# Kernel tuning notes

Measured on AMD Instinct MI355X. Metric: run time of the kernel, lower is better.

Reference implementation:

```python
import jax, jax.numpy as jnp
import numpy as np

H = 256          # hidden_size
L = 2            # num_layers
K = 4            # khops
R = 128          # relation_num
N_NODES = 20000
N_EDGES = 160000
N_LG_EDGES = 640000


def setup_inputs() -> dict:
    key = jax.random.key(0)
    ks = iter(jax.random.split(key, 40))
    def nrm(shape, s=1.0):
        return jax.random.normal(next(ks), shape, dtype=jnp.float32) * s
    w = 1.0 / float(np.sqrt(H))
    return {
        "x": nrm((N_NODES, H)),
        "edge_feat": jax.random.randint(next(ks), (N_EDGES,), 0, R),
        "edge_index_g": jax.random.randint(next(ks), (2, N_EDGES), 0, N_NODES),
        "edge_index_lg": jax.random.randint(next(ks), (2, N_LG_EDGES), 0, N_EDGES),
        "rel_embed": nrm((R, H)),
        # per-layer, per-core (0=node update, 1=edge update) parameter stacks
        "w_self": nrm((L, 2, H, H), w), "b_self": jnp.zeros((L, 2, H), jnp.float32),
        "w_khop": nrm((L, 2, K, H, H), w), "b_khop": jnp.zeros((L, 2, K, H), jnp.float32),
        "w_fuse": nrm((L, 2, H, H), w), "b_fuse": jnp.zeros((L, 2, H), jnp.float32),
        "w_ff1": nrm((L, 2, H, 4 * H), w), "b_ff1": jnp.zeros((L, 2, 4 * H), jnp.float32),
        "w_ff2": nrm((L, 2, 4 * H, H), 1.0 / float(np.sqrt(4 * H))), "b_ff2": jnp.zeros((L, 2, H), jnp.float32),
        "ln1_g": jnp.ones((L, 2, H), jnp.float32), "ln1_b": jnp.zeros((L, 2, H), jnp.float32),
        "ln2_g": jnp.ones((L, 2, H), jnp.float32), "ln2_b": jnp.zeros((L, 2, H), jnp.float32),
    }


def _layernorm(x, g, b, eps=1e-5):
    m = jnp.mean(x, axis=-1, keepdims=True)
    v = jnp.var(x, axis=-1, keepdims=True)
    return (x - m) * jax.lax.rsqrt(v + eps) * g + b


def _core(p, src, dst, x, fused):
    """LGNNCore.forward (eval mode, dropout never applied in core)."""
    (ws, bs, wk, bk, wf, bf, w1, b1, w2, b2, g1, c1, g2, c2) = p
    n = x.shape[0]
    prev = x @ ws + bs
    # k-hop copy_src + sum aggregation, each hop gets its own linear
    z = x
    kh = jnp.zeros_like(prev)
    for i in range(wk.shape[0]):
        z = jax.ops.segment_sum(z[src], dst, num_segments=n)
        kh = kh + z @ wk[i] + bk[i]
    edge = fused @ wf + bf
    out = jax.nn.gelu(prev + kh + edge, approximate=False)
    out = _layernorm(x + out, g1, c1)
    ffn = jax.nn.gelu(out @ w1 + b1, approximate=False) @ w2 + b2
    return _layernorm(out + ffn, g2, c2)


def reference(x, edge_feat, edge_index_g, edge_index_lg, rel_embed,
              w_self, b_self, w_khop, b_khop, w_fuse, b_fuse,
              w_ff1, b_ff1, w_ff2, b_ff2, ln1_g, ln1_b, ln2_g, ln2_b):
    lg_x = rel_embed[edge_feat]                       # [n_edges, H]
    src_g, dst_g = edge_index_g[0], edge_index_g[1]
    src_l, dst_l = edge_index_lg[0], edge_index_lg[1]
    n_nodes = x.shape[0]
    for l in range(w_self.shape[0]):
        def pick(c):
            return (w_self[l, c], b_self[l, c], w_khop[l, c], b_khop[l, c],
                    w_fuse[l, c], b_fuse[l, c], w_ff1[l, c], b_ff1[l, c],
                    w_ff2[l, c], b_ff2[l, c], ln1_g[l, c], ln1_b[l, c],
                    ln2_g[l, c], ln2_b[l, c])
        # pmpd @ lg_x : scatter each edge feature to both of its endpoints
        fused_nodes = (jax.ops.segment_sum(lg_x, src_g, num_segments=n_nodes)
                       + jax.ops.segment_sum(lg_x, dst_g, num_segments=n_nodes))
        # pmpd^T @ x : gather both endpoint node features per edge
        fused_edges = x[src_g] + x[dst_g]
        new_x = _core(pick(0), src_g, dst_g, x, fused_nodes)
        new_lg_x = _core(pick(1), src_l, dst_l, lg_x, fused_edges)
        x, lg_x = new_x, new_lg_x
    return x, lg_x
```

## Files before the change

### kernel.cpp

```cpp
#include <hip/hip_runtime.h>

typedef __bf16 bf16;
typedef __attribute__((ext_vector_type(8))) __bf16 bf16x8;
typedef __attribute__((ext_vector_type(4))) __bf16 bf16x4;
typedef __attribute__((ext_vector_type(4))) float f32x4;

#define HD 256
#define GEMM_GELU 2

__device__ __forceinline__ float gelu_f(float x) {
  float x2 = x * x;
  float u = 1.5957691216057308f * x * fmaf(0.044715f, x2, 1.0f);
  float e = __expf(-u);
  return x / (1.0f + e);
}

__device__ __forceinline__ void gload_lds16(const void* g, void* l) {
  __builtin_amdgcn_global_load_lds(
      (const __attribute__((address_space(1))) unsigned int*)g,
      (__attribute__((address_space(3))) unsigned int*)l, 16, 0, 0);
}

__global__ __launch_bounds__(256) void gemm_k(
    const bf16* __restrict__ A, const bf16* __restrict__ Wt,
    const float* __restrict__ bias, bf16* __restrict__ C,
    int M, int Kd, int lda, int ldc, int flags)
{
  __shared__ __align__(16) bf16 sA[2][128 * 64];
  __shared__ __align__(16) bf16 sB[2][128 * 64];
  const int t = threadIdx.x;
  const int lane = t & 63, w = t >> 6;
  const int n0 = blockIdx.x * 128, m0 = blockIdx.y * 128;
  const int wr = w >> 1, wc = w & 1;
  const int lm = lane & 15, quad = lane >> 4;

  const int rowl = lane >> 3;
  const int gcl = (lane & 7) ^ rowl;
  const bool full = (m0 + 128 <= M);

  const char* pa = (const char*)(A + (size_t)(m0 + w * 32 + rowl) * lda) + gcl * 16;
  const char* pb = (const char*)(Wt + (size_t)(n0 + w * 32 + rowl) * Kd) + gcl * 16;
  const size_t stepA = (size_t)8 * lda * 2;
  const size_t stepB = (size_t)8 * Kd * 2;

  f32x4 acc[4][4];
#pragma unroll
  for (int i = 0; i < 4; i++)
#pragma unroll
    for (int j = 0; j < 4; j++)
#pragma unroll
      for (int r = 0; r < 4; r++) acc[i][j][r] = 0.f;

  const int nk = Kd >> 6;

  auto stage = [&](bf16* SA, bf16* SB, int kt) {
    size_t ko = (size_t)kt * 128;
#pragma unroll
    for (int i = 0; i < 4; i++)
      gload_lds16(pa + i * stepA + ko, SA + w * 2048 + i * 512);
#pragma unroll
    for (int i = 0; i < 4; i++)
      gload_lds16(pb + i * stepB + ko, SB + w * 2048 + i * 512);
  };

  auto compute = [&](const bf16* SA, const bf16* SB) {
#pragma unroll
    for (int s = 0; s < 2; s++) {
      const int soff = ((s * 4 + quad) ^ (lm & 7)) * 8;
      bf16x8 af[4], bv[4];
#pragma unroll
      for (int i = 0; i < 4; i++) af[i] = *(const bf16x8*)(SA + (wr * 64 + i * 16 + lm) * 64 + soff);
#pragma unroll
      for (int j = 0; j < 4; j++) bv[j] = *(const bf16x8*)(SB + (wc * 64 + j * 16 + lm) * 64 + soff);
#pragma unroll
      for (int i = 0; i < 4; i++)
#pragma unroll
        for (int j = 0; j < 4; j++)
          acc[i][j] = __builtin_amdgcn_mfma_f32_16x16x32_bf16(bv[j], af[i], acc[i][j], 0, 0, 0);
    }
  };

  if (full) {
    stage(sA[0], sB[0], 0);
    for (int kt = 0; kt < nk; ++kt) {
      int nxt = kt + 1;
      if (nxt < nk) {
        stage(sA[nxt & 1], sB[nxt & 1], nxt);
        asm volatile("s_waitcnt vmcnt(8)" ::: "memory");
      } else {
        asm volatile("s_waitcnt vmcnt(0)" ::: "memory");
      }
      __builtin_amdgcn_s_barrier();
      asm volatile("" ::: "memory");
      compute(sA[kt & 1], sB[kt & 1]);
      __builtin_amdgcn_s_barrier();
      asm volatile("" ::: "memory");
    }
  } else {
    for (int kt = 0; kt < nk; ++kt) {
      size_t ko = (size_t)kt * 128;
#pragma unroll
      for (int c = 0; c < 4; c++) {
        int sid = t + c * 256;
        int row = sid >> 3, sc = sid & 7;
        int gc = sc ^ (row & 7);
        int gr = m0 + row;
        bf16x8 va;
#pragma unroll
        for (int q = 0; q < 8; q++) va[q] = (bf16)0.f;
        if (gr < M) va = *(const bf16x8*)((const char*)(A + (size_t)gr * lda) + ko + gc * 16);
        *(bf16x8*)(sA[0] + row * 64 + sc * 8) = va;
      }
#pragma unroll
      for (int i = 0; i < 4; i++)
        gload_lds16(pb + i * stepB + ko, sB[0] + w * 2048 + i * 512);
      __syncthreads();
      compute(sA[0], sB[0]);
      __syncthreads();
    }
  }

  float4 bia[4];
#pragma unroll
  for (int j = 0; j < 4; j++)
    bia[j] = *(const float4*)(bias + n0 + wc * 64 + j * 16 + quad * 4);
#pragma unroll
  for (int i = 0; i < 4; i++) {
    int gr = m0 + wr * 64 + i * 16 + lm;
    if (gr < M) {
      bf16* crow = C + (size_t)gr * ldc;
#pragma unroll
      for (int j = 0; j < 4; j++) {
        int gc = n0 + wc * 64 + j * 16 + quad * 4;
        float v0 = acc[i][j][0] + bia[j].x;
        float v1 = acc[i][j][1] + bia[j].y;
        float v2 = acc[i][j][2] + bia[j].z;
        float v3 = acc[i][j][3] + bia[j].w;
        if (flags & GEMM_GELU) {
          v0 = gelu_f(v0); v1 = gelu_f(v1); v2 = gelu_f(v2); v3 = gelu_f(v3);
        }
        bf16x4 o = {(bf16)v0, (bf16)v1, (bf16)v2, (bf16)v3};
        *(bf16x4*)(crow + gc) = o;
      }
    }
  }
}

__global__ __launch_bounds__(256) void segsum_k(
    const int* __restrict__ offs, const int* __restrict__ cols,
    const bf16* __restrict__ in, int ldin, bf16* __restrict__ out, int ldout, int nseg)
{
  int wid = threadIdx.x >> 6, lane = threadIdx.x & 63;
  int seg = blockIdx.x * 4 + wid;
  if (seg >= nseg) return;
  int b = offs[seg], e = offs[seg + 1];
  float a0 = 0.f, a1 = 0.f, a2 = 0.f, a3 = 0.f;
  for (int i = b; i < e; i++) {
    int c = cols[i];
    bf16x4 v = *(const bf16x4*)(in + (size_t)c * ldin + lane * 4);
    a0 += (float)v.x; a1 += (float)v.y; a2 += (float)v.z; a3 += (float)v.w;
  }
  bf16x4 o = {(bf16)a0, (bf16)a1, (bf16)a2, (bf16)a3};
  *(bf16x4*)(out + (size_t)seg * ldout + lane * 4) = o;
}

__global__ __launch_bounds__(256) void ln_k(
    const bf16* __restrict__ X, int ldx, const bf16* __restrict__ A,
    const float* __restrict__ gam, const float* __restrict__ bet,
    bf16* __restrict__ outb, float* __restrict__ outf, int M, int apply_gelu)
{
  int wid = threadIdx.x >> 6, lane = threadIdx.x & 63;
  int row = blockIdx.x * 4 + wid;
  if (row >= M) return;
  size_t xbase = (size_t)row * ldx + lane * 4;
  size_t abase = (size_t)row * HD + lane * 4;
  bf16x4 xv = *(const bf16x4*)(X + xbase);
  bf16x4 av = *(const bf16x4*)(A + abase);
  float s0, s1, s2, s3;
  if (apply_gelu) {
    s0 = (float)xv.x + gelu_f((float)av.x);
    s1 = (float)xv.y + gelu_f((float)av.y);
    s2 = (float)xv.z + gelu_f((float)av.z);
    s3 = (float)xv.w + gelu_f((float)av.w);
  } else {
    s0 = (float)xv.x + (float)av.x;
    s1 = (float)xv.y + (float)av.y;
    s2 = (float)xv.z + (float)av.z;
    s3 = (float)xv.w + (float)av.w;
  }
  float sum = s0 + s1 + s2 + s3;
#pragma unroll
  for (int o = 32; o; o >>= 1) sum += __shfl_xor(sum, o, 64);
  float mean = sum * (1.0f / 256.0f);
  float d0 = s0 - mean, d1 = s1 - mean, d2 = s2 - mean, d3 = s3 - mean;
  float vs = d0 * d0 + d1 * d1 + d2 * d2 + d3 * d3;
#pragma unroll
  for (int o = 32; o; o >>= 1) vs += __shfl_xor(vs, o, 64);
  float rstd = rsqrtf(vs * (1.0f / 256.0f) + 1e-5f);
  float4 g = *(const float4*)(gam + lane * 4);
  float4 bb = *(const float4*)(bet + lane * 4);
  float y0 = d0 * rstd * g.x + bb.x;
  float y1 = d1 * rstd * g.y + bb.y;
  float y2 = d2 * rstd * g.z + bb.z;
  float y3 = d3 * rstd * g.w + bb.w;
  if (outb) {
    bf16x4 o = {(bf16)y0, (bf16)y1, (bf16)y2, (bf16)y3};
    *(bf16x4*)(outb + xbase) = o;
  }
  if (outf) {
    float4 o = {y0, y1, y2, y3};
    *(float4*)(outf + abase) = o;
  }
}

__global__ __launch_bounds__(256) void gather_rel_k(
    const int* __restrict__ feat, const float* __restrict__ rel,
    bf16* __restrict__ out, int ldout, int NE)
{
  int wid = threadIdx.x >> 6, lane = threadIdx.x & 63;
  int e = blockIdx.x * 4 + wid;
  if (e >= NE) return;
  int f = feat[e];
  float4 v = *(const float4*)(rel + (size_t)f * HD + lane * 4);
  bf16x4 o = {(bf16)v.x, (bf16)v.y, (bf16)v.z, (bf16)v.w};
  *(bf16x4*)(out + (size_t)e * ldout + lane * 4) = o;
}

__global__ __launch_bounds__(256) void gather2_k(
    const int* __restrict__ src, const int* __restrict__ dst,
    const bf16* __restrict__ x, int ldx, bf16* __restrict__ out, int ldout, int NE)
{
  int wid = threadIdx.x >> 6, lane = threadIdx.x & 63;
  int e = blockIdx.x * 4 + wid;
  if (e >= NE) return;
  int s = src[e], d = dst[e];
  bf16x4 a = *(const bf16x4*)(x + (size_t)s * ldx + lane * 4);
  bf16x4 b = *(const bf16x4*)(x + (size_t)d * ldx + lane * 4);
  bf16x4 o = {(bf16)((float)a.x + (float)b.x), (bf16)((float)a.y + (float)b.y),
              (bf16)((float)a.z + (float)b.z), (bf16)((float)a.w + (float)b.w)};
  *(bf16x4*)(out + (size_t)e * ldout + lane * 4) = o;
}

__global__ __launch_bounds__(256) void f2b_k(const float* __restrict__ in,
                                             bf16* __restrict__ out, int ldout, int M) {
  int wid = threadIdx.x >> 6, lane = threadIdx.x & 63;
  int row = blockIdx.x * 4 + wid;
  if (row >= M) return;
  float4 v = *(const float4*)(in + (size_t)row * HD + lane * 4);
  bf16x4 o = {(bf16)v.x, (bf16)v.y, (bf16)v.z, (bf16)v.w};
  *(bf16x4*)(out + (size_t)row * ldout + lane * 4) = o;
}

__global__ __launch_bounds__(256) void wtrans_k(const float* __restrict__ in, bf16* __restrict__ out,
                                                int Kd, int Nd) {
  size_t moff = (size_t)blockIdx.y * Kd * Nd;
  int id = blockIdx.x * 256 + threadIdx.x;
  if (id >= Kd * Nd) return;
  int n = id / Kd, k = id - n * Kd;
  out[moff + id] = (bf16)in[moff + (size_t)k * Nd + n];
}

__global__ __launch_bounds__(256) void wcat_k(const float* __restrict__ ws, const float* __restrict__ wk,
                                              const float* __restrict__ wf, bf16* __restrict__ out,
                                              int KH, int CW) {
  int mi = blockIdx.y;
  int id = blockIdx.x * 256 + threadIdx.x;
  if (id >= HD * CW) return;
  int n = id / CW, k = id - n * CW;
  int s = k >> 8, kk = k & 255;
  float v;
  if (s == 0)       v = ws[((size_t)mi * HD + kk) * HD + n];
  else if (s <= KH) v = wk[(((size_t)mi * KH + (s - 1)) * HD + kk) * HD + n];
  else              v = wf[((size_t)mi * HD + kk) * HD + n];
  out[(size_t)mi * HD * CW + id] = (bf16)v;
}

__global__ __launch_bounds__(256) void bcat_k(const float* __restrict__ bs, const float* __restrict__ bk,
                                              const float* __restrict__ bf, float* __restrict__ out, int KH) {
  int mi = blockIdx.x, n = threadIdx.x;
  float v = bs[(size_t)mi * HD + n] + bf[(size_t)mi * HD + n];
  for (int i = 0; i < KH; i++) v += bk[((size_t)mi * KH + i) * HD + n];
  out[(size_t)mi * HD + n] = v;
}

__global__ __launch_bounds__(256) void count_k(const int* __restrict__ keys, int n, int* __restrict__ cnt) {
  int i = blockIdx.x * 256 + threadIdx.x;
  if (i < n) atomicAdd(&cnt[keys[i]], 1);
}
__global__ __launch_bounds__(256) void scan1_k(const int* __restrict__ in, int* __restrict__ out,
                                               int* __restrict__ bsum, int n) {
  __shared__ int sh[256];
  int t = threadIdx.x;
  int i0 = blockIdx.x * 1024 + t * 4;
  int v0 = (i0 < n) ? in[i0] : 0;
  int v1 = (i0 + 1 < n) ? in[i0 + 1] : 0;
  int v2 = (i0 + 2 < n) ? in[i0 + 2] : 0;
  int v3 = (i0 + 3 < n) ? in[i0 + 3] : 0;
  int tsum = v0 + v1 + v2 + v3;
  sh[t] = tsum;
  __syncthreads();
  for (int o = 1; o < 256; o <<= 1) {
    int x = (t >= o) ? sh[t - o] : 0;
    __syncthreads();
    sh[t] += x;
    __syncthreads();
  }
  int e0 = sh[t] - tsum;
  if (t == 255) bsum[blockIdx.x] = sh[255];
  if (i0 < n) out[i0] = e0;
  e0 += v0;
  if (i0 + 1 < n) out[i0 + 1] = e0;
  e0 += v1;
  if (i0 + 2 < n) out[i0 + 2] = e0;
  e0 += v2;
  if (i0 + 3 < n) out[i0 + 3] = e0;
}
__global__ void scan2_k(int* bsum, int nb, int* total) {
  if (threadIdx.x == 0 && blockIdx.x == 0) {
    int acc = 0;
    for (int i = 0; i < nb; i++) { int v = bsum[i]; bsum[i] = acc; acc += v; }
    *total = acc;
  }
}
__global__ __launch_bounds__(256) void scan3_k(int* out, const int* bsum, int n) {
  int i = blockIdx.x * 256 + threadIdx.x;
  if (i < n) out[i] += bsum[i >> 10];
}
__global__ __launch_bounds__(256) void fill_k(const int* __restrict__ keys, const int* __restrict__ vals,
                                              int n, int modE, int* __restrict__ cursor, int* __restrict__ cols) {
  int i = blockIdx.x * 256 + threadIdx.x;
  if (i >= n) return;
  int pos = atomicAdd(&cursor[keys[i]], 1);
  cols[pos] = vals ? vals[i] : (i < modE ? i : i - modE);
}

extern "C" void kernel_launch(void* const* d_in, const int* in_sizes, int n_in,
                              void* d_out, int out_size, void* d_ws, size_t ws_size,
                              hipStream_t stream)
{
  const float* x_in      = (const float*)d_in[0];
  const int*   edge_feat = (const int*)d_in[1];
  const int*   eig       = (const int*)d_in[2];
  const int*   eil       = (const int*)d_in[3];
  const float* rel       = (const float*)d_in[4];
  const float* w_self = (const float*)d_in[5];
  const float* b_self = (const float*)d_in[6];
  const float* w_khop = (const float*)d_in[7];
  const float* b_khop = (const float*)d_in[8];
  const float* w_fuse = (const float*)d_in[9];
  const float* b_fuse = (const float*)d_in[10];
  const float* w_ff1  = (const float*)d_in[11];
  const float* b_ff1  = (const float*)d_in[12];
  const float* w_ff2  = (const float*)d_in[13];
  const float* b_ff2  = (const float*)d_in[14];
  const float* ln1_g  = (const float*)d_in[15];
  const float* ln1_b  = (const float*)d_in[16];
  const float* ln2_g  = (const float*)d_in[17];
  const float* ln2_b  = (const float*)d_in[18];

  const int NN = in_sizes[0] / HD;
  const int NE = in_sizes[1];
  const int NL = in_sizes[3] / 2;
  const int L  = in_sizes[5] / (2 * HD * HD);
  const int KH = in_sizes[7] / (L * 2 * HD * HD);
  const int CW = (KH + 2) * HD;

  char* p = (char*)d_ws;
  auto alloc = [&](size_t bytes) -> void* {
    void* r = (void*)p;
    p += (bytes + 255) & ~(size_t)255;
    return r;
  };

  bf16* n_cat  = (bf16*)alloc((size_t)NN * CW * 2);
  bf16* lg_cat = (bf16*)alloc((size_t)NE * CW * 2);
  bf16* acc_n  = (bf16*)alloc((size_t)NN * HD * 2);
  bf16* acc_e  = (bf16*)alloc((size_t)NE * HD * 2);

  bf16*  wcat_t = (bf16*)alloc((size_t)L * 2 * HD * CW * 2);
  float* bcat   = (float*)alloc((size_t)L * 2 * HD * 4);
  bf16*  wff1_t = (bf16*)alloc((size_t)L * 2 * HD * 4 * HD * 2);
  bf16*  wff2_t = (bf16*)alloc((size_t)L * 2 * HD * 4 * HD * 2);

  int* inc_offs = (int*)alloc((size_t)(NN + 1) * 4);
  int* inc_cur  = (int*)alloc((size_t)NN * 4);
  int* inc_cols = (int*)alloc((size_t)2 * NE * 4);
  int* ng_offs  = (int*)alloc((size_t)(NN + 1) * 4);
  int* ng_cur   = (int*)alloc((size_t)NN * 4);
  int* ng_cols  = (int*)alloc((size_t)NE * 4);
  int* lg_offs  = (int*)alloc((size_t)(NE + 1) * 4);
  int* lg_cur   = (int*)alloc((size_t)NE * 4);
  int* lg_cols  = (int*)alloc((size_t)NL * 4);
  int* bsum     = (int*)alloc(3 * 256 * 4);

  wcat_k<<<dim3((HD * CW + 255) / 256, L * 2), 256, 0, stream>>>(w_self, w_khop, w_fuse, wcat_t, KH, CW);
  bcat_k<<<L * 2, 256, 0, stream>>>(b_self, b_khop, b_fuse, bcat, KH);
  wtrans_k<<<dim3((HD * 4 * HD + 255) / 256, L * 2), 256, 0, stream>>>(w_ff1, wff1_t, HD, 4 * HD);
  wtrans_k<<<dim3((HD * 4 * HD + 255) / 256, L * 2), 256, 0, stream>>>(w_ff2, wff2_t, 4 * HD, HD);

  f2b_k<<<(NN + 3) / 4, 256, 0, stream>>>(x_in, n_cat, CW, NN);
  gather_rel_k<<<(NE + 3) / 4, 256, 0, stream>>>(edge_feat, rel, lg_cat, CW, NE);

  auto build_csr = [&](const int* keys, int nkeys, const int* vals, int modE,
                       int nseg, int* offs, int* cur, int* cols, int* bs) {
    int nb = (nseg + 1023) / 1024;
    hipMemsetAsync(offs, 0, (size_t)(nseg + 1) * 4, stream);
    count_k<<<(nkeys + 255) / 256, 256, 0, stream>>>(keys, nkeys, offs);
    scan1_k<<<nb, 256, 0, stream>>>(offs, offs, bs, nseg);
    scan2_k<<<1, 1, 0, stream>>>(bs, nb, offs + nseg);
    scan3_k<<<(nseg + 255) / 256, 256, 0, stream>>>(offs, bs, nseg);
    hipMemcpyAsync(cur, offs, (size_t)nseg * 4, hipMemcpyDeviceToDevice, stream);
    fill_k<<<(nkeys + 255) / 256, 256, 0, stream>>>(keys, vals, nkeys, modE, cur, cols);
  };
  build_csr(eig, 2 * NE, nullptr, NE, NN, inc_offs, inc_cur, inc_cols, bsum);
  build_csr(eig + NE, NE, eig, 0, NN, ng_offs, ng_cur, ng_cols, bsum + 256);
  build_csr(eil + NL, NL, eil, 0, NE, lg_offs, lg_cur, lg_cols, bsum + 512);

  float* out_x  = (float*)d_out;
  float* out_lg = (float*)d_out + (size_t)NN * HD;

  auto run_core = [&](bf16* cat, bf16* accb, const int* coffs, const int* ccols,
                      int M, int l, int c, float* outf) {
    size_t mi = (size_t)(l * 2 + c);
    int mb = (M + 127) / 128;
    for (int i = 1; i <= KH; i++)
      segsum_k<<<(M + 3) / 4, 256, 0, stream>>>(coffs, ccols, cat + (size_t)(i - 1) * HD, CW,
                                                cat + (size_t)i * HD, CW, M);
    gemm_k<<<dim3(2, mb), 256, 0, stream>>>(cat, wcat_t + mi * HD * CW, bcat + mi * HD,
                                            accb, M, CW, CW, HD, 0);
    ln_k<<<(M + 3) / 4, 256, 0, stream>>>(cat, CW, accb, ln1_g + mi * HD, ln1_b + mi * HD,
                                          cat, (float*)nullptr, M, 1);
    bf16* hid = cat + HD;
    int FC = (M > 40000) ? 40000 : M;
    for (int c0 = 0; c0 < M; c0 += FC) {
      int mc = (M - c0 < FC) ? (M - c0) : FC;
      int mbc = (mc + 127) / 128;
      gemm_k<<<dim3(8, mbc), 256, 0, stream>>>(cat + (size_t)c0 * CW, wff1_t + mi * HD * 4 * HD,
                                               b_ff1 + mi * 4 * HD, hid, mc, HD, CW, CW, GEMM_GELU);
      gemm_k<<<dim3(2, mbc), 256, 0, stream>>>(hid, wff2_t + mi * 4 * HD * HD, b_ff2 + mi * HD,
                                               accb + (size_t)c0 * HD, mc, 4 * HD, CW, HD, 0);
    }
    ln_k<<<(M + 3) / 4, 256, 0, stream>>>(cat, CW, accb, ln2_g + mi * HD, ln2_b + mi * HD,
                                          cat, outf, M, 0);
  };

  for (int l = 0; l < L; l++) {
    segsum_k<<<(NN + 3) / 4, 256, 0, stream>>>(inc_offs, inc_cols, lg_cat, CW,
                                               n_cat + (size_t)(KH + 1) * HD, CW, NN);
    gather2_k<<<(NE + 3) / 4, 256, 0, stream>>>(eig, eig + NE, n_cat, CW,
                                                lg_cat + (size_t)(KH + 1) * HD, CW, NE);
    run_core(n_cat, acc_n, ng_offs, ng_cols, NN, l, 0, (l == L - 1) ? out_x : nullptr);
    run_core(lg_cat, acc_e, lg_offs, lg_cols, NE, l, 1, (l == L - 1) ? out_lg : nullptr);
  }
}
```

Baseline: 3.293 ms.

## Give each wave a private A buffer and load B fragments into registers

The GEMM no longer shares LDS tiles across the block. Each wave stages its own 64-row A slice into a private double buffer and loads its B (weight) fragments straight from global memory into registers, which removes both block-wide barriers per K step. The catch is redundant traffic: A rows are loaded twice, once by each of the two waves sharing a row group, and B rows are reloaded from global by each wave instead of being shared through LDS. Register pressure also goes up because B is double-buffered in VGPRs.

Result: slower. 4.136 ms (+25.6%).

```diff
diff --git a/kernel.cpp b/kernel.cpp
--- a/kernel.cpp
+++ b/kernel.cpp
@@ -26,22 +26,22 @@
     const float* __restrict__ bias, bf16* __restrict__ C,
     int M, int Kd, int lda, int ldc, int flags)
 {
-  __shared__ __align__(16) bf16 sA[2][128 * 64];
-  __shared__ __align__(16) bf16 sB[2][128 * 64];
+  __shared__ __align__(16) bf16 sA[2][4][64 * 64];
   const int t = threadIdx.x;
   const int lane = t & 63, w = t >> 6;
   const int n0 = blockIdx.x * 128, m0 = blockIdx.y * 128;
   const int wr = w >> 1, wc = w & 1;
   const int lm = lane & 15, quad = lane >> 4;
-
   const int rowl = lane >> 3;
   const int gcl = (lane & 7) ^ rowl;
   const bool full = (m0 + 128 <= M);
 
-  const char* pa = (const char*)(A + (size_t)(m0 + w * 32 + rowl) * lda) + gcl * 16;
-  const char* pb = (const char*)(Wt + (size_t)(n0 + w * 32 + rowl) * Kd) + gcl * 16;
+  const char* pa = (const char*)(A + (size_t)(m0 + wr * 64 + rowl) * lda) + gcl * 16;
   const size_t stepA = (size_t)8 * lda * 2;
-  const size_t stepB = (size_t)8 * Kd * 2;
+  const bf16* pbL = Wt + (size_t)(n0 + wc * 64 + lm) * Kd + quad * 8;
+
+  bf16* buf0 = &sA[0][w][0];
+  bf16* buf1 = &sA[1][w][0];
 
   f32x4 acc[4][4];
 #pragma unroll
@@ -53,70 +53,63 @@
 
   const int nk = Kd >> 6;
 
-  auto stage = [&](bf16* SA, bf16* SB, int kt) {
+  bf16x8 bA[2][4], bB[2][4];
+
+  auto loadB = [&](int kt, bf16x8 (&bb)[2][4]) {
+#pragma unroll
+    for (int s = 0; s < 2; s++)
+#pragma unroll
+      for (int j = 0; j < 4; j++)
+        bb[s][j] = *(const bf16x8*)(pbL + (size_t)j * 16 * Kd + (size_t)kt * 64 + s * 32);
+  };
+  auto stageA = [&](bf16* buf, int kt) {
     size_t ko = (size_t)kt * 128;
 #pragma unroll
-    for (int i = 0; i < 4; i++)
-      gload_lds16(pa + i * stepA + ko, SA + w * 2048 + i * 512);
-#pragma unroll
-    for (int i = 0; i < 4; i++)
-      gload_lds16(pb + i * stepB + ko, SB + w * 2048 + i * 512);
-  };
-
-  auto compute = [&](const bf16* SA, const bf16* SB) {
+    for (int i = 0; i < 8; i++)
+      gload_lds16(pa + i * stepA + ko, buf + i * 512);
+  };
+  auto compute = [&](const bf16* buf, bf16x8 (&bb)[2][4]) {
 #pragma unroll
     for (int s = 0; s < 2; s++) {
-      const int soff = ((s * 4 + quad) ^ (lm & 7)) * 8;
-      bf16x8 af[4], bv[4];
-#pragma unroll
-      for (int i = 0; i < 4; i++) af[i] = *(const bf16x8*)(SA + (wr * 64 + i * 16 + lm) * 64 + soff);
-#pragma unroll
-      for (int j = 0; j < 4; j++) bv[j] = *(const bf16x8*)(SB + (wc * 64 + j * 16 + lm) * 64 + soff);
+      bf16x8 af[4];
 #pragma unroll
       for (int i = 0; i < 4; i++)
+        af[i] = *(const bf16x8*)(buf + (i * 16 + lm) * 64 + ((s * 4 + quad) ^ (lm & 7)) * 8);
+#pragma unroll
+      for (int i = 0; i < 4; i++)
 #pragma unroll
         for (int j = 0; j < 4; j++)
-          acc[i][j] = __builtin_amdgcn_mfma_f32_16x16x32_bf16(bv[j], af[i], acc[i][j], 0, 0, 0);
+          acc[i][j] = __builtin_amdgcn_mfma_f32_16x16x32_bf16(bb[s][j], af[i], acc[i][j], 0, 0, 0);
     }
   };
 
   if (full) {
-    stage(sA[0], sB[0], 0);
-    for (int kt = 0; kt < nk; ++kt) {
-      int nxt = kt + 1;
-      if (nxt < nk) {
-        stage(sA[nxt & 1], sB[nxt & 1], nxt);
-        asm volatile("s_waitcnt vmcnt(8)" ::: "memory");
-      } else {
-        asm volatile("s_waitcnt vmcnt(0)" ::: "memory");
-      }
-      __builtin_amdgcn_s_barrier();
-      asm volatile("" ::: "memory");
-      compute(sA[kt & 1], sB[kt & 1]);
-      __builtin_amdgcn_s_barrier();
-      asm volatile("" ::: "memory");
+    loadB(0, bA); stageA(buf0, 0);
+    loadB(1, bB); stageA(buf1, 1);
+    for (int kt = 0; kt < nk; kt += 2) {
+      if (kt + 1 < nk) { asm volatile("s_waitcnt vmcnt(16)" ::: "memory"); }
+      else             { asm volatile("s_waitcnt vmcnt(0)" ::: "memory"); }
+      compute(buf0, bA);
+      if (kt + 2 < nk) { loadB(kt + 2, bA); stageA(buf0, kt + 2); }
+      if (kt + 2 < nk) { asm volatile("s_waitcnt vmcnt(16)" ::: "memory"); }
+      else             { asm volatile("s_waitcnt vmcnt(0)" ::: "memory"); }
+      compute(buf1, bB);
+      if (kt + 3 < nk) { loadB(kt + 3, bB); stageA(buf1, kt + 3); }
     }
   } else {
     for (int kt = 0; kt < nk; ++kt) {
-      size_t ko = (size_t)kt * 128;
-#pragma unroll
-      for (int c = 0; c < 4; c++) {
-        int sid = t + c * 256;
-        int row = sid >> 3, sc = sid & 7;
-        int gc = sc ^ (row & 7);
-        int gr = m0 + row;
+      size_t ko = (size_t)kt * 64;
+      loadB(kt, bA);
+#pragma unroll
+      for (int i = 0; i < 8; i++) {
+        int gr = m0 + wr * 64 + i * 8 + rowl;
         bf16x8 va;
 #pragma unroll
         for (int q = 0; q < 8; q++) va[q] = (bf16)0.f;
-        if (gr < M) va = *(const bf16x8*)((const char*)(A + (size_t)gr * lda) + ko + gc * 16);
-        *(bf16x8*)(sA[0] + row * 64 + sc * 8) = va;
+        if (gr < M) va = *(const bf16x8*)(A + (size_t)gr * lda + ko + gcl * 8);
+        *(bf16x8*)(buf0 + i * 512 + lane * 8) = va;
       }
-#pragma unroll
-      for (int i = 0; i < 4; i++)
-        gload_lds16(pb + i * stepB + ko, sB[0] + w * 2048 + i * 512);
-      __syncthreads();
-      compute(sA[0], sB[0]);
-      __syncthreads();
+      compute(buf0, bA);
     }
   }
 
```

## Fuse residual+GELU+LayerNorm into GEMM epilogue with 64x256 tiles

Applied to the files above, without the earlier changes.

Retiles the GEMM to 64x256 so each block owns full 256-wide rows, which lets residual add, GELU and LayerNorm run in the epilogue using a cross-wave LDS reduction. The separate ln_k kernel and the acc buffers are removed. The segment-sum loop is also unrolled by four to issue more gathers at once. The cost is larger LDS for B and fewer blocks for the N=256 GEMMs. It also writes in place into cat, which the epilogue reads as the residual.

New measurement: 3.038 ms. 7.7% less time.

```diff
diff --git a/kernel.cpp b/kernel.cpp
--- a/kernel.cpp
+++ b/kernel.cpp
@@ -7,6 +7,9 @@
 
 #define HD 256
 #define GEMM_GELU 2
+#define GEMM_LN1  4
+#define GEMM_LN2  8
+#define GEMM_F32  16
 
 __device__ __forceinline__ float gelu_f(float x) {
   float x2 = x * x;
@@ -24,22 +27,22 @@
 __global__ __launch_bounds__(256) void gemm_k(
     const bf16* __restrict__ A, const bf16* __restrict__ Wt,
     const float* __restrict__ bias, bf16* __restrict__ C,
+    const bf16* __restrict__ Xres, const float* __restrict__ gam,
+    const float* __restrict__ bet, float* __restrict__ outf,
     int M, int Kd, int lda, int ldc, int flags)
 {
-  __shared__ __align__(16) bf16 sA[2][128 * 64];
-  __shared__ __align__(16) bf16 sB[2][128 * 64];
+  __shared__ __align__(16) bf16 sA[2][64 * 64];
+  __shared__ __align__(16) bf16 sB[2][256 * 64];
   const int t = threadIdx.x;
   const int lane = t & 63, w = t >> 6;
-  const int n0 = blockIdx.x * 128, m0 = blockIdx.y * 128;
-  const int wr = w >> 1, wc = w & 1;
+  const int n0 = blockIdx.x * 256, m0 = blockIdx.y * 64;
   const int lm = lane & 15, quad = lane >> 4;
-
   const int rowl = lane >> 3;
   const int gcl = (lane & 7) ^ rowl;
-  const bool full = (m0 + 128 <= M);
-
-  const char* pa = (const char*)(A + (size_t)(m0 + w * 32 + rowl) * lda) + gcl * 16;
-  const char* pb = (const char*)(Wt + (size_t)(n0 + w * 32 + rowl) * Kd) + gcl * 16;
+  const bool full = (m0 + 64 <= M);
+
+  const char* pa = (const char*)(A + (size_t)(m0 + w * 16 + rowl) * lda) + gcl * 16;
+  const char* pb = (const char*)(Wt + (size_t)(n0 + w * 64 + rowl) * Kd) + gcl * 16;
   const size_t stepA = (size_t)8 * lda * 2;
   const size_t stepB = (size_t)8 * Kd * 2;
 
@@ -55,23 +58,24 @@
 
   auto stage = [&](bf16* SA, bf16* SB, int kt) {
     size_t ko = (size_t)kt * 128;
-#pragma unroll
-    for (int i = 0; i < 4; i++)
-      gload_lds16(pa + i * stepA + ko, SA + w * 2048 + i * 512);
-#pragma unroll
-    for (int i = 0; i < 4; i++)
-      gload_lds16(pb + i * stepB + ko, SB + w * 2048 + i * 512);
+    gload_lds16(pa + ko, SA + w * 1024);
+    gload_lds16(pa + stepA + ko, SA + w * 1024 + 512);
+#pragma unroll
+    for (int i = 0; i < 8; i++)
+      gload_lds16(pb + i * stepB + ko, SB + w * 4096 + i * 512);
   };
 
   auto compute = [&](const bf16* SA, const bf16* SB) {
 #pragma unroll
     for (int s = 0; s < 2; s++) {
-      const int soff = ((s * 4 + quad) ^ (lm & 7)) * 8;
+      const int so = ((s * 4 + quad) ^ (lm & 7)) * 8;
       bf16x8 af[4], bv[4];
 #pragma unroll
-      for (int i = 0; i < 4; i++) af[i] = *(const bf16x8*)(SA + (wr * 64 + i * 16 + lm) * 64 + soff);
-#pragma unroll
-      for (int j = 0; j < 4; j++) bv[j] = *(const bf16x8*)(SB + (wc * 64 + j * 16 + lm) * 64 + soff);
+      for (int i = 0; i < 4; i++)
+        af[i] = *(const bf16x8*)(SA + (i * 16 + lm) * 64 + so);
+#pragma unroll
+      for (int j = 0; j < 4; j++)
+        bv[j] = *(const bf16x8*)(SB + (w * 64 + j * 16 + lm) * 64 + so);
 #pragma unroll
       for (int i = 0; i < 4; i++)
 #pragma unroll
@@ -83,10 +87,9 @@
   if (full) {
     stage(sA[0], sB[0], 0);
     for (int kt = 0; kt < nk; ++kt) {
-      int nxt = kt + 1;
-      if (nxt < nk) {
-        stage(sA[nxt & 1], sB[nxt & 1], nxt);
-        asm volatile("s_waitcnt vmcnt(8)" ::: "memory");
+      if (kt + 1 < nk) {
+        stage(sA[(kt + 1) & 1], sB[(kt + 1) & 1], kt + 1);
+        asm volatile("s_waitcnt vmcnt(10)" ::: "memory");
       } else {
         asm volatile("s_waitcnt vmcnt(0)" ::: "memory");
       }
@@ -98,49 +101,104 @@
     }
   } else {
     for (int kt = 0; kt < nk; ++kt) {
-      size_t ko = (size_t)kt * 128;
-#pragma unroll
-      for (int c = 0; c < 4; c++) {
-        int sid = t + c * 256;
-        int row = sid >> 3, sc = sid & 7;
-        int gc = sc ^ (row & 7);
+      size_t koe = (size_t)kt * 64;
+#pragma unroll
+      for (int i = 0; i < 2; i++) {
+        int row = w * 16 + i * 8 + rowl;
         int gr = m0 + row;
         bf16x8 va;
 #pragma unroll
         for (int q = 0; q < 8; q++) va[q] = (bf16)0.f;
-        if (gr < M) va = *(const bf16x8*)((const char*)(A + (size_t)gr * lda) + ko + gc * 16);
-        *(bf16x8*)(sA[0] + row * 64 + sc * 8) = va;
-      }
-#pragma unroll
-      for (int i = 0; i < 4; i++)
-        gload_lds16(pb + i * stepB + ko, sB[0] + w * 2048 + i * 512);
+        if (gr < M) va = *(const bf16x8*)(A + (size_t)gr * lda + koe + gcl * 8);
+        *(bf16x8*)(sA[0] + row * 64 + (lane & 7) * 8) = va;
+      }
+#pragma unroll
+      for (int i = 0; i < 8; i++)
+        gload_lds16(pb + i * stepB + koe * 2, sB[0] + w * 4096 + i * 512);
       __syncthreads();
       compute(sA[0], sB[0]);
       __syncthreads();
     }
   }
 
-  float4 bia[4];
+  f32x4 bia[4];
 #pragma unroll
   for (int j = 0; j < 4; j++)
-    bia[j] = *(const float4*)(bias + n0 + wc * 64 + j * 16 + quad * 4);
-#pragma unroll
-  for (int i = 0; i < 4; i++) {
-    int gr = m0 + wr * 64 + i * 16 + lm;
-    if (gr < M) {
-      bf16* crow = C + (size_t)gr * ldc;
+    bia[j] = *(const f32x4*)(bias + n0 + w * 64 + j * 16 + quad * 4);
+
+  if (flags & (GEMM_LN1 | GEMM_LN2)) {
+    float* ps = (float*)&sA[0][0];
+    float* pq = ps + 64 * 16;
+#pragma unroll
+    for (int i = 0; i < 4; i++) {
+      int gr = m0 + i * 16 + lm;
+      float lsum = 0.f, lsq = 0.f;
 #pragma unroll
       for (int j = 0; j < 4; j++) {
-        int gc = n0 + wc * 64 + j * 16 + quad * 4;
-        float v0 = acc[i][j][0] + bia[j].x;
-        float v1 = acc[i][j][1] + bia[j].y;
-        float v2 = acc[i][j][2] + bia[j].z;
-        float v3 = acc[i][j][3] + bia[j].w;
-        if (flags & GEMM_GELU) {
-          v0 = gelu_f(v0); v1 = gelu_f(v1); v2 = gelu_f(v2); v3 = gelu_f(v3);
+        bf16x4 xv = {(bf16)0.f, (bf16)0.f, (bf16)0.f, (bf16)0.f};
+        if (gr < M) xv = *(const bf16x4*)(Xres + (size_t)gr * ldc + w * 64 + j * 16 + quad * 4);
+#pragma unroll
+        for (int r = 0; r < 4; r++) {
+          float v = acc[i][j][r] + bia[j][r];
+          if (flags & GEMM_LN1) v = gelu_f(v);
+          v += (float)xv[r];
+          acc[i][j][r] = v;
+          lsum += v; lsq += v * v;
         }
-        bf16x4 o = {(bf16)v0, (bf16)v1, (bf16)v2, (bf16)v3};
-        *(bf16x4*)(crow + gc) = o;
+      }
+      ps[(i * 16 + lm) * 16 + w * 4 + quad] = lsum;
+      pq[(i * 16 + lm) * 16 + w * 4 + quad] = lsq;
+    }
+    __syncthreads();
+#pragma unroll
+    for (int i = 0; i < 4; i++) {
+      int gr = m0 + i * 16 + lm;
+      float sum = 0.f, sq = 0.f;
+#pragma unroll
+      for (int k = 0; k < 16; k++) {
+        sum += ps[(i * 16 + lm) * 16 + k];
+        sq  += pq[(i * 16 + lm) * 16 + k];
+      }
+      float mean = sum * (1.0f / 256.0f);
+      float var = sq * (1.0f / 256.0f) - mean * mean;
+      float rstd = rsqrtf(fmaxf(var, 0.f) + 1e-5f);
+      if (gr < M) {
+        bf16* crow = C + (size_t)gr * ldc;
+        float* frow = (flags & GEMM_F32) ? (outf + (size_t)gr * HD) : nullptr;
+#pragma unroll
+        for (int j = 0; j < 4; j++) {
+          int gc = w * 64 + j * 16 + quad * 4;
+          f32x4 g = *(const f32x4*)(gam + gc);
+          f32x4 bb = *(const f32x4*)(bet + gc);
+          float y0 = (acc[i][j][0] - mean) * rstd * g[0] + bb[0];
+          float y1 = (acc[i][j][1] - mean) * rstd * g[1] + bb[1];
+          float y2 = (acc[i][j][2] - mean) * rstd * g[2] + bb[2];
+          float y3 = (acc[i][j][3] - mean) * rstd * g[3] + bb[3];
+          bf16x4 o = {(bf16)y0, (bf16)y1, (bf16)y2, (bf16)y3};
+          *(bf16x4*)(crow + gc) = o;
+          if (frow) { f32x4 fo = {y0, y1, y2, y3}; *(f32x4*)(frow + gc) = fo; }
+        }
+      }
+    }
+  } else {
+#pragma unroll
+    for (int i = 0; i < 4; i++) {
+      int gr = m0 + i * 16 + lm;
+      if (gr < M) {
+        bf16* crow = C + (size_t)gr * ldc;
+#pragma unroll
+        for (int j = 0; j < 4; j++) {
+          int gc = n0 + w * 64 + j * 16 + quad * 4;
+          float v0 = acc[i][j][0] + bia[j][0];
+          float v1 = acc[i][j][1] + bia[j][1];
+          float v2 = acc[i][j][2] + bia[j][2];
+          float v3 = acc[i][j][3] + bia[j][3];
+          if (flags & GEMM_GELU) {
+            v0 = gelu_f(v0); v1 = gelu_f(v1); v2 = gelu_f(v2); v3 = gelu_f(v3);
+          }
+          bf16x4 o = {(bf16)v0, (bf16)v1, (bf16)v2, (bf16)v3};
+          *(bf16x4*)(crow + gc) = o;
+        }
       }
     }
   }
@@ -155,62 +213,25 @@
   if (seg >= nseg) return;
   int b = offs[seg], e = offs[seg + 1];
   float a0 = 0.f, a1 = 0.f, a2 = 0.f, a3 = 0.f;
-  for (int i = b; i < e; i++) {
+  int i = b;
+  for (; i + 4 <= e; i += 4) {
+    int c0 = cols[i], c1 = cols[i + 1], c2 = cols[i + 2], c3 = cols[i + 3];
+    bf16x4 v0 = *(const bf16x4*)(in + (size_t)c0 * ldin + lane * 4);
+    bf16x4 v1 = *(const bf16x4*)(in + (size_t)c1 * ldin + lane * 4);
+    bf16x4 v2 = *(const bf16x4*)(in + (size_t)c2 * ldin + lane * 4);
+    bf16x4 v3 = *(const bf16x4*)(in + (size_t)c3 * ldin + lane * 4);
+    a0 += (float)v0.x; a1 += (float)v0.y; a2 += (float)v0.z; a3 += (float)v0.w;
+    a0 += (float)v1.x; a1 += (float)v1.y; a2 += (float)v1.z; a3 += (float)v1.w;
+    a0 += (float)v2.x; a1 += (float)v2.y; a2 += (float)v2.z; a3 += (float)v2.w;
+    a0 += (float)v3.x; a1 += (float)v3.y; a2 += (float)v3.z; a3 += (float)v3.w;
+  }
+  for (; i < e; i++) {
     int c = cols[i];
     bf16x4 v = *(const bf16x4*)(in + (size_t)c * ldin + lane * 4);
     a0 += (float)v.x; a1 += (float)v.y; a2 += (float)v.z; a3 += (float)v.w;
   }
   bf16x4 o = {(bf16)a0, (bf16)a1, (bf16)a2, (bf16)a3};
   *(bf16x4*)(out + (size_t)seg * ldout + lane * 4) = o;
-}
-
-__global__ __launch_bounds__(256) void ln_k(
-    const bf16* __restrict__ X, int ldx, const bf16* __restrict__ A,
-    const float* __restrict__ gam, const float* __restrict__ bet,
-    bf16* __restrict__ outb, float* __restrict__ outf, int M, int apply_gelu)
-{
-  int wid = threadIdx.x >> 6, lane = threadIdx.x & 63;
-  int row = blockIdx.x * 4 + wid;
-  if (row >= M) return;
-  size_t xbase = (size_t)row * ldx + lane * 4;
-  size_t abase = (size_t)row * HD + lane * 4;
-  bf16x4 xv = *(const bf16x4*)(X + xbase);
-  bf16x4 av = *(const bf16x4*)(A + abase);
-  float s0, s1, s2, s3;
-  if (apply_gelu) {
-    s0 = (float)xv.x + gelu_f((float)av.x);
-    s1 = (float)xv.y + gelu_f((float)av.y);
-    s2 = (float)xv.z + gelu_f((float)av.z);
-    s3 = (float)xv.w + gelu_f((float)av.w);
-  } else {
-    s0 = (float)xv.x + (float)av.x;
-    s1 = (float)xv.y + (float)av.y;
-    s2 = (float)xv.z + (float)av.z;
-    s3 = (float)xv.w + (float)av.w;
-  }
-  float sum = s0 + s1 + s2 + s3;
-#pragma unroll
-  for (int o = 32; o; o >>= 1) sum += __shfl_xor(sum, o, 64);
-  float mean = sum * (1.0f / 256.0f);
-  float d0 = s0 - mean, d1 = s1 - mean, d2 = s2 - mean, d3 = s3 - mean;
-  float vs = d0 * d0 + d1 * d1 + d2 * d2 + d3 * d3;
-#pragma unroll
-  for (int o = 32; o; o >>= 1) vs += __shfl_xor(vs, o, 64);
-  float rstd = rsqrtf(vs * (1.0f / 256.0f) + 1e-5f);
-  float4 g = *(const float4*)(gam + lane * 4);
-  float4 bb = *(const float4*)(bet + lane * 4);
-  float y0 = d0 * rstd * g.x + bb.x;
-  float y1 = d1 * rstd * g.y + bb.y;
-  float y2 = d2 * rstd * g.z + bb.z;
-  float y3 = d3 * rstd * g.w + bb.w;
-  if (outb) {
-    bf16x4 o = {(bf16)y0, (bf16)y1, (bf16)y2, (bf16)y3};
-    *(bf16x4*)(outb + xbase) = o;
-  }
-  if (outf) {
-    float4 o = {y0, y1, y2, y3};
-    *(float4*)(outf + abase) = o;
-  }
 }
 
 __global__ __launch_bounds__(256) void gather_rel_k(
@@ -374,8 +395,6 @@
 
   bf16* n_cat  = (bf16*)alloc((size_t)NN * CW * 2);
   bf16* lg_cat = (bf16*)alloc((size_t)NE * CW * 2);
-  bf16* acc_n  = (bf16*)alloc((size_t)NN * HD * 2);
-  bf16* acc_e  = (bf16*)alloc((size_t)NE * HD * 2);
 
   bf16*  wcat_t = (bf16*)alloc((size_t)L * 2 * HD * CW * 2);
   float* bcat   = (float*)alloc((size_t)L * 2 * HD * 4);
@@ -419,29 +438,29 @@
   float* out_x  = (float*)d_out;
   float* out_lg = (float*)d_out + (size_t)NN * HD;
 
-  auto run_core = [&](bf16* cat, bf16* accb, const int* coffs, const int* ccols,
+  auto run_core = [&](bf16* cat, const int* coffs, const int* ccols,
                       int M, int l, int c, float* outf) {
     size_t mi = (size_t)(l * 2 + c);
-    int mb = (M + 127) / 128;
     for (int i = 1; i <= KH; i++)
       segsum_k<<<(M + 3) / 4, 256, 0, stream>>>(coffs, ccols, cat + (size_t)(i - 1) * HD, CW,
                                                 cat + (size_t)i * HD, CW, M);
-    gemm_k<<<dim3(2, mb), 256, 0, stream>>>(cat, wcat_t + mi * HD * CW, bcat + mi * HD,
-                                            accb, M, CW, CW, HD, 0);
-    ln_k<<<(M + 3) / 4, 256, 0, stream>>>(cat, CW, accb, ln1_g + mi * HD, ln1_b + mi * HD,
-                                          cat, (float*)nullptr, M, 1);
+    gemm_k<<<dim3(1, (M + 63) / 64), 256, 0, stream>>>(
+        cat, wcat_t + mi * HD * CW, bcat + mi * HD, cat,
+        cat, ln1_g + mi * HD, ln1_b + mi * HD, nullptr,
+        M, CW, CW, CW, GEMM_LN1);
     bf16* hid = cat + HD;
     int FC = (M > 40000) ? 40000 : M;
     for (int c0 = 0; c0 < M; c0 += FC) {
       int mc = (M - c0 < FC) ? (M - c0) : FC;
-      int mbc = (mc + 127) / 128;
-      gemm_k<<<dim3(8, mbc), 256, 0, stream>>>(cat + (size_t)c0 * CW, wff1_t + mi * HD * 4 * HD,
-                                               b_ff1 + mi * 4 * HD, hid, mc, HD, CW, CW, GEMM_GELU);
-      gemm_k<<<dim3(2, mbc), 256, 0, stream>>>(hid, wff2_t + mi * 4 * HD * HD, b_ff2 + mi * HD,
-                                               accb + (size_t)c0 * HD, mc, 4 * HD, CW, HD, 0);
-    }
-    ln_k<<<(M + 3) / 4, 256, 0, stream>>>(cat, CW, accb, ln2_g + mi * HD, ln2_b + mi * HD,
-                                          cat, outf, M, 0);
+      gemm_k<<<dim3(4, (mc + 63) / 64), 256, 0, stream>>>(
+          cat + (size_t)c0 * CW, wff1_t + mi * HD * 4 * HD, b_ff1 + mi * 4 * HD, hid,
+          nullptr, nullptr, nullptr, nullptr, mc, HD, CW, CW, GEMM_GELU);
+      gemm_k<<<dim3(1, (mc + 63) / 64), 256, 0, stream>>>(
+          hid, wff2_t + mi * 4 * HD * HD, b_ff2 + mi * HD, cat + (size_t)c0 * CW,
+          cat + (size_t)c0 * CW, ln2_g + mi * HD, ln2_b + mi * HD,
+          outf ? outf + (size_t)c0 * HD : nullptr,
+          mc, 4 * HD, CW, CW, GEMM_LN2 | (outf ? GEMM_F32 : 0));
+    }
   };
 
   for (int l = 0; l < L; l++) {
@@ -449,7 +468,7 @@
                                                n_cat + (size_t)(KH + 1) * HD, CW, NN);
     gather2_k<<<(NE + 3) / 4, 256, 0, stream>>>(eig, eig + NE, n_cat, CW,
                                                 lg_cat + (size_t)(KH + 1) * HD, CW, NE);
-    run_core(n_cat, acc_n, ng_offs, ng_cols, NN, l, 0, (l == L - 1) ? out_x : nullptr);
-    run_core(lg_cat, acc_e, lg_offs, lg_cols, NE, l, 1, (l == L - 1) ? out_lg : nullptr);
-  }
-}
+    run_core(n_cat, ng_offs, ng_cols, NN, l, 0, (l == L - 1) ? out_x : nullptr);
+    run_core(lg_cat, lg_offs, lg_cols, NE, l, 1, (l == L - 1) ? out_lg : nullptr);
+  }
+}
```
